# Performance work log

Measured on AMD Instinct MI355X. Metric: run time of the kernel, lower is better.

Reference implementation:

```python
import jax, jax.numpy as jnp
import numpy as np

B, S, E = 2, 2048, 2048
H, G = 16, 4
HD = E // H  # 128 head dim


def setup_inputs() -> dict:
    key = jax.random.key(0)
    k1, k2, k3, k4 = jax.random.split(key, 4)
    x = jax.random.normal(k1, (B, S, E), dtype=jnp.float32)
    mask = jnp.zeros((B, 1, S, S), dtype=jnp.float32)
    # torch nn.Linear weights stored as [in, out] for x @ W
    W1 = jax.random.normal(k2, (E, 2 * G * HD), dtype=jnp.float32) * 0.02
    W2 = jax.random.normal(k3, (E, E), dtype=jnp.float32) * 0.02
    W3 = jax.random.normal(k4, (E, E), dtype=jnp.float32) * 0.02
    return {"x": x, "mask": mask, "W1": W1, "W2": W2, "W3": W3}


def reference(x, mask, W1, W2, W3):
    b, s, e_model = x.shape
    hd = e_model // H
    # linear_1 -> rearrange 'b s (n g e) -> n b g s e'
    kv = (x @ W1).reshape(b, s, 2, G, hd).transpose(2, 0, 3, 1, 4)
    k, v = kv[0], kv[1]  # [b, g, s, e]
    # linear_2 -> 'b t (h e) -> b h t e'
    q = (x @ W2).reshape(b, s, H, hd).transpose(0, 2, 1, 3)  # [b, h, t, e]
    # NOTE: g is summed out here, exactly as in the source einsum (no sqrt scaling)
    score = jnp.einsum('bhte,bgse->bhts', q, k)
    score = jax.nn.softmax(score + mask, axis=-1)
    out = jnp.einsum('bhts,bgse->bthe', score, v)  # g summed again
    out = out.reshape(b, s, e_model)
    return out @ W3
```

## Files before the change

### kernel.cpp

```cpp
#include <hip/hip_runtime.h>
#include <cstdint>

#define S_LEN 2048
#define EMB   2048
#define NHEAD 16
#define HDIM  128
#define NFUSE 2304
#define LOG2E 1.4426950408889634f

typedef __attribute__((ext_vector_type(8))) _Float16 h8;
typedef __attribute__((ext_vector_type(4))) _Float16 h4;
typedef __attribute__((ext_vector_type(8))) short short8;
typedef __attribute__((ext_vector_type(4))) short short4v;
typedef __attribute__((ext_vector_type(4))) float f32x4;
typedef unsigned int u32;

__device__ inline short f2bf(float x) {
  union { float f; uint32_t u; } v; v.f = x;
  uint32_t r = v.u + 0x7fffu + ((v.u >> 16) & 1u);
  return (short)(r >> 16);
}
__device__ inline float bf2f(short b) {
  union { uint32_t u; float f; } v; v.u = ((uint32_t)(uint16_t)b) << 16;
  return v.f;
}
__device__ inline float fexp2(float x) {
  float r;
  __asm__ volatile("v_exp_f32 %0, %1" : "=v"(r) : "v"(x));
  return r;
}
__device__ inline u32 pkrtz(float a, float b) {
  u32 r;
  __asm__ volatile("v_cvt_pkrtz_f16_f32 %0, %1, %2" : "=v"(r) : "v"(a), "v"(b));
  return r;
}
__device__ inline void glds16(const void* g, void* l) {
  __builtin_amdgcn_global_load_lds(
      (const __attribute__((address_space(1))) u32*)g,
      (__attribute__((address_space(3))) u32*)l, 16, 0, 0);
}

__global__ __launch_bounds__(256) void reduce_w1_kernel(
    const float* __restrict__ W1, float* __restrict__ Wkv) {
  int idx = blockIdx.x * 256 + threadIdx.x;
  int i = idx >> 8;
  int c = idx & 255;
  int base = (c < 128) ? c : (c + 384);
  const float* r = W1 + (size_t)i * 1024 + base;
  Wkv[idx] = (r[0] + r[128]) + (r[256] + r[384]);
}

__global__ __launch_bounds__(256) void cvt_x_kernel(
    const float* __restrict__ src, _Float16* __restrict__ dst) {
  size_t idx = (size_t)blockIdx.x * 256 + threadIdx.x;
  float4 v = *(const float4*)(src + idx * 4);
  h4 o;
  o[0] = (_Float16)v.x; o[1] = (_Float16)v.y;
  o[2] = (_Float16)v.z; o[3] = (_Float16)v.w;
  *(h4*)(dst + idx * 4) = o;
}

__global__ __launch_bounds__(256) void cvt_mask_kernel(
    const float* __restrict__ src, short* __restrict__ dst) {
  size_t idx = (size_t)blockIdx.x * 256 + threadIdx.x;
  float4 v = *(const float4*)(src + idx * 4);
  short4v o;
  o[0] = f2bf(v.x * LOG2E); o[1] = f2bf(v.y * LOG2E);
  o[2] = f2bf(v.z * LOG2E); o[3] = f2bf(v.w * LOG2E);
  *(short4v*)(dst + idx * 4) = o;
}

__global__ __launch_bounds__(256) void transpose_f16_kernel(
    const float* __restrict__ W, _Float16* __restrict__ T, int K, int N) {
  __shared__ float Tt[64][65];
  const int tid = threadIdx.x;
  const int k0 = blockIdx.y * 64, n0 = blockIdx.x * 64;
  {
    int r = tid >> 2, c0 = (tid & 3) * 16;
    const float* src = W + (size_t)(k0 + r) * N + n0 + c0;
#pragma unroll
    for (int j = 0; j < 4; ++j) {
      float4 v = *(const float4*)(src + 4 * j);
      Tt[r][c0 + 4 * j + 0] = v.x; Tt[r][c0 + 4 * j + 1] = v.y;
      Tt[r][c0 + 4 * j + 2] = v.z; Tt[r][c0 + 4 * j + 3] = v.w;
    }
  }
  __syncthreads();
  {
    int n = tid >> 2, kc = (tid & 3) * 16;
    h8 o0, o1;
#pragma unroll
    for (int i = 0; i < 8; ++i) {
      o0[i] = (_Float16)Tt[kc + i][n];
      o1[i] = (_Float16)Tt[kc + 8 + i][n];
    }
    size_t off = (size_t)(n0 + n) * K + k0 + kc;
    *(h8*)(T + off) = o0;
    *(h8*)(T + off + 8) = o1;
  }
}

template <bool QSCALE>
__global__ __launch_bounds__(256, 3) void gemm_f16(
    const _Float16* __restrict__ A, const _Float16* __restrict__ Bt,
    float* __restrict__ C, _Float16* __restrict__ Cf,
    int M, int N, int K, int qlim) {
  extern __shared__ char smraw[];
  _Float16* sm = (_Float16*)smraw;
  const int BUFS = 8192;

  const int tid  = threadIdx.x;
  const int w    = tid >> 6;
  const int lane = tid & 63;
  const int quad = lane >> 4, col16 = lane & 15;
  const int row0 = blockIdx.y * 128, col0 = blockIdx.x * 128;
  const float esc = (col0 < qlim) ? LOG2E : 1.0f;

  const int srow  = w * 32 + (lane >> 2);
  const int kpart = (lane & 3) * 8;
  const _Float16* pA0 = A + (size_t)(row0 + srow) * K + kpart;
  const _Float16* pA1 = pA0 + (size_t)16 * K;
  const _Float16* pB0 = Bt + (size_t)(col0 + srow) * K + kpart;
  const _Float16* pB1 = pB0 + (size_t)16 * K;

  const int oA0 = (w * 32) * 32, oA1 = (w * 32 + 16) * 32;
  const int oB0 = 4096 + (w * 32) * 32, oB1 = 4096 + (w * 32 + 16) * 32;

#define STAGE_GEMM(bo)                                                        \
  do {                                                                        \
    glds16(pA0, sm + (bo) + oA0); glds16(pA1, sm + (bo) + oA1);               \
    glds16(pB0, sm + (bo) + oB0); glds16(pB1, sm + (bo) + oB1);               \
    pA0 += 32; pA1 += 32; pB0 += 32; pB1 += 32;                               \
  } while (0)

  f32x4 acc[2][8];
#pragma unroll
  for (int mt = 0; mt < 2; ++mt)
#pragma unroll
    for (int nt = 0; nt < 8; ++nt) {
      acc[mt][nt][0] = 0.f; acc[mt][nt][1] = 0.f;
      acc[mt][nt][2] = 0.f; acc[mt][nt][3] = 0.f;
    }

  const int nchunk = K >> 5;
  int bo = 0;
  STAGE_GEMM(0);

#pragma unroll 1
  for (int c = 0; c < nchunk; ++c) {
    if (c + 1 < nchunk) {
      STAGE_GEMM(bo ^ BUFS);
      __asm__ volatile("s_waitcnt vmcnt(4)" ::: "memory");
    } else {
      __asm__ volatile("s_waitcnt vmcnt(0)" ::: "memory");
    }
    __builtin_amdgcn_s_barrier();

    const _Float16* AS = sm + bo;
    const _Float16* BS = sm + bo + 4096;

    h8 af[2];
#pragma unroll
    for (int mt = 0; mt < 2; ++mt)
      af[mt] = *(const h8*)&AS[(w * 32 + mt * 16 + col16) * 32 + quad * 8];
#pragma unroll
    for (int nt = 0; nt < 8; ++nt) {
      h8 b8 = *(const h8*)&BS[(nt * 16 + col16) * 32 + quad * 8];
#pragma unroll
      for (int mt = 0; mt < 2; ++mt)
        acc[mt][nt] = __builtin_amdgcn_mfma_f32_16x16x32_f16(af[mt], b8, acc[mt][nt], 0, 0, 0);
    }
    __builtin_amdgcn_s_barrier();
    bo ^= BUFS;
  }
#undef STAGE_GEMM

#pragma unroll
  for (int mt = 0; mt < 2; ++mt)
#pragma unroll
    for (int nt = 0; nt < 8; ++nt)
#pragma unroll
      for (int r = 0; r < 4; ++r) {
        int row = row0 + w * 32 + mt * 16 + quad * 4 + r;
        int col = col0 + nt * 16 + col16;
        float v = acc[mt][nt][r];
        if constexpr (QSCALE) {
          Cf[(size_t)row * N + col] = (_Float16)(v * esc);
        } else {
          C[(size_t)row * N + col] = v;
        }
      }
}

__global__ __launch_bounds__(256) void build_vt(
    const short* __restrict__ QKh, short* __restrict__ VT) {
  __shared__ short T[64][136];
  const int tid = threadIdx.x;
  const int gs = blockIdx.x * 64;
  const int b = gs >> 11;
  const int s = gs & 2047;
  {
    int r = tid >> 2, c0 = (tid & 3) * 32;
    const short* src = QKh + (size_t)(gs + r) * NFUSE + 2176 + c0;
#pragma unroll
    for (int j = 0; j < 4; ++j)
      *(short8*)&T[r][c0 + 8 * j] = *(const short8*)(src + 8 * j);
  }
  __syncthreads();
  {
    int d = tid >> 1, c = (tid & 1) * 32;
    short* dst = VT + (size_t)(b * HDIM + d) * S_LEN + s + c;
#pragma unroll
    for (int jo = 0; jo < 4; ++jo) {
      short8 o;
#pragma unroll
      for (int i = 0; i < 8; ++i) o[i] = T[c + jo * 8 + i][d];
      *(short8*)(dst + jo * 8) = o;
    }
  }
}

__global__ __launch_bounds__(256, 2) void flash_f16(
    const _Float16* __restrict__ QKf, const _Float16* __restrict__ VT,
    const short* __restrict__ maskb, _Float16* __restrict__ AO) {
  __shared__ _Float16 KS[64 * 128];
  __shared__ _Float16 VtS[128 * 64];
  __shared__ _Float16 PsS[2 * 4 * 16 * 64];
  __shared__ short    MkS[4 * 32 * 64];

  const int tid   = threadIdx.x;
  const int w     = tid >> 6;
  const int lane  = tid & 63;
  const int quad  = lane >> 4;
  const int col16 = lane & 15;
  const int xq    = col16 & 7;
  const int bh = blockIdx.y, b = bh >> 4, h = bh & 15;
  const int t0 = blockIdx.x * 128;

  const int jr = lane >> 4;
  const int kg = lane & 15;
  const int vr = lane >> 3;
  const int vg = lane & 7;

  _Float16* myK = KS + w * 2048;
  _Float16* myV = VtS + w * 2048;
  short*    myM = MkS + w * 2048;

  h8 qf[2][4];
#pragma unroll
  for (int t = 0; t < 2; ++t) {
#pragma unroll
    for (int j = 0; j < 4; ++j) {
      int rl = 4 * j + jr;
      int gq = kg ^ (rl & 7);
      size_t go = (size_t)(b * S_LEN + t0 + 64 * t + 16 * w + rl) * NFUSE
                + h * HDIM + gq * 8;
      glds16(QKf + go, myK + j * 512);
    }
    __asm__ volatile("s_waitcnt vmcnt(0)" ::: "memory");
#pragma unroll
    for (int c = 0; c < 4; ++c)
      qf[t][c] = *(const h8*)&myK[col16 * 128 + (((c * 4 + quad) ^ xq) * 8)];
    __asm__ volatile("s_waitcnt lgkmcnt(0)" ::: "memory");
  }

  const _Float16* Kbase = QKf + (size_t)b * S_LEN * NFUSE + 2048;
  const _Float16* Vbase = VT + (size_t)b * HDIM * S_LEN;
  const short*    Mbase = maskb + (size_t)b * S_LEN * S_LEN;
  u32 offK[4], offV[4], offM[4];
#pragma unroll
  for (int j = 0; j < 4; ++j) {
    int rl = 4 * j + jr;
    offK[j] = (u32)(16 * w + rl) * NFUSE + (u32)((kg ^ (rl & 7)) * 8);
    int dl = 32 * w + 8 * j + vr;
    offV[j] = (u32)dl * S_LEN + (u32)((vg ^ (vr & 7)) * 8);
    int mrw = j * 8 + (lane >> 3);
    int mq  = t0 + 64 * (mrw >> 4) + 16 * w + (mrw & 15);
    offM[j] = (u32)mq * S_LEN + (u32)(((lane & 7) ^ (mrw & 7)) * 8);
  }

#pragma unroll
  for (int j = 0; j < 4; ++j) glds16(Kbase + offK[j], myK + j * 512);
#pragma unroll
  for (int j = 0; j < 4; ++j) glds16(Mbase + offM[j], myM + j * 512);
#pragma unroll
  for (int j = 0; j < 4; ++j) glds16(Vbase + offV[j], myV + j * 512);
#pragma unroll
  for (int j = 0; j < 4; ++j) {
    offK[j] += 64 * NFUSE; offM[j] += 64; offV[j] += 64;
  }

  f32x4 oacc[2][8];
#pragma unroll
  for (int t = 0; t < 2; ++t)
#pragma unroll
    for (int d = 0; d < 8; ++d) {
      oacc[t][d][0] = 0.f; oacc[t][d][1] = 0.f;
      oacc[t][d][2] = 0.f; oacc[t][d][3] = 0.f;
    }
  float mrow[2] = {-3.0e38f, -3.0e38f};
  float lrow[2] = {0.f, 0.f};

#pragma unroll 1
  for (int it = 0; it < S_LEN / 64; ++it) {
    __asm__ volatile("s_waitcnt vmcnt(8)" ::: "memory");
    __builtin_amdgcn_s_barrier();

    f32x4 sacc[2][4];
#pragma unroll
    for (int t = 0; t < 2; ++t)
#pragma unroll
      for (int nt = 0; nt < 4; ++nt) {
        sacc[t][nt][0] = 0.f; sacc[t][nt][1] = 0.f;
        sacc[t][nt][2] = 0.f; sacc[t][nt][3] = 0.f;
      }
    __builtin_amdgcn_s_setprio(1);
#pragma unroll
    for (int c = 0; c < 4; ++c)
#pragma unroll
      for (int nt = 0; nt < 4; ++nt) {
        h8 k8 = *(const h8*)&KS[(nt * 16 + col16) * 128 + (((c * 4 + quad) ^ xq) * 8)];
#pragma unroll
        for (int t = 0; t < 2; ++t)
          sacc[t][nt] = __builtin_amdgcn_mfma_f32_16x16x32_f16(k8, qf[t][c], sacc[t][nt], 0, 0, 0);
      }
    __builtin_amdgcn_s_setprio(0);

    __asm__ volatile("s_waitcnt vmcnt(0)" ::: "memory");
    short4v msk[2][4];
#pragma unroll
    for (int t = 0; t < 2; ++t)
#pragma unroll
      for (int nt = 0; nt < 4; ++nt)
        msk[t][nt] = *(const short4v*)
            &myM[(t * 16 + col16) * 64 + (((quad + nt * 4) ^ (xq << 1)) << 2)];
    __asm__ volatile("s_waitcnt lgkmcnt(0)" ::: "memory");
    __builtin_amdgcn_s_barrier();

    if (it + 1 < S_LEN / 64) {
#pragma unroll
      for (int j = 0; j < 4; ++j) glds16(Kbase + offK[j], myK + j * 512);
#pragma unroll
      for (int j = 0; j < 4; ++j) glds16(Mbase + offM[j], myM + j * 512);
#pragma unroll
      for (int j = 0; j < 4; ++j) { offK[j] += 64 * NFUSE; offM[j] += 64; }
    }

#pragma unroll
    for (int t = 0; t < 2; ++t) {
      float vv[4][4];
#pragma unroll
      for (int nt = 0; nt < 4; ++nt)
#pragma unroll
        for (int r = 0; r < 4; ++r)
          vv[nt][r] = sacc[t][nt][r] + bf2f(msk[t][nt][r]);
      float mx = vv[0][0];
#pragma unroll
      for (int nt = 0; nt < 4; ++nt)
#pragma unroll
        for (int r = 0; r < 4; ++r) mx = fmaxf(mx, vv[nt][r]);
      mx = fmaxf(mx, __shfl_xor(mx, 16));
      mx = fmaxf(mx, __shfl_xor(mx, 32));

      float nm = fmaxf(mrow[t], mx);
      if (__all(mx - mrow[t] <= 8.0f)) {
        nm = mrow[t];
      } else {
        float al = fexp2(mrow[t] - nm);
        lrow[t] *= al;
#pragma unroll
        for (int d = 0; d < 8; ++d) {
          oacc[t][d][0] *= al; oacc[t][d][1] *= al;
          oacc[t][d][2] *= al; oacc[t][d][3] *= al;
        }
        mrow[t] = nm;
      }

      float ps = 0.f;
      u32 pk0[4], pk1[4];
#pragma unroll
      for (int nt = 0; nt < 4; ++nt) {
        float p0 = fexp2(vv[nt][0] - nm);
        float p1 = fexp2(vv[nt][1] - nm);
        float p2 = fexp2(vv[nt][2] - nm);
        float p3 = fexp2(vv[nt][3] - nm);
        ps += (p0 + p1) + (p2 + p3);
        pk0[nt] = pkrtz(p0, p1);
        pk1[nt] = pkrtz(p2, p3);
      }
      ps += __shfl_xor(ps, 16);
      ps += __shfl_xor(ps, 32);
      lrow[t] += ps;

      int pbase = ((t * 4 + w) * 16 + col16) * 64 + (quad & 1) * 4;
#pragma unroll
      for (int nt = 0; nt < 4; ++nt) {
        uint2 pv2; pv2.x = pk0[nt]; pv2.y = pk1[nt];
        *(uint2*)&PsS[pbase + (((2 * nt + (quad >> 1)) ^ xq) * 8)] = pv2;
      }
    }

    __asm__ volatile("s_waitcnt lgkmcnt(0)" ::: "memory");
    h8 pa[2][2];
#pragma unroll
    for (int t = 0; t < 2; ++t) {
      int pb = ((t * 4 + w) * 16 + col16) * 64;
      pa[t][0] = *(const h8*)&PsS[pb + ((quad ^ xq) * 8)];
      pa[t][1] = *(const h8*)&PsS[pb + (((4 + quad) ^ xq) * 8)];
    }
    __builtin_amdgcn_s_setprio(1);
#pragma unroll
    for (int d = 0; d < 8; ++d) {
      int vo = (d * 16 + col16) * 64;
      h8 vb0 = *(const h8*)&VtS[vo + ((quad ^ xq) * 8)];
      h8 vb1 = *(const h8*)&VtS[vo + (((4 + quad) ^ xq) * 8)];
#pragma unroll
      for (int t = 0; t < 2; ++t) {
        oacc[t][d] = __builtin_amdgcn_mfma_f32_16x16x32_f16(vb0, pa[t][0], oacc[t][d], 0, 0, 0);
        oacc[t][d] = __builtin_amdgcn_mfma_f32_16x16x32_f16(vb1, pa[t][1], oacc[t][d], 0, 0, 0);
      }
    }
    __builtin_amdgcn_s_setprio(0);

    __builtin_amdgcn_s_barrier();
    if (it + 1 < S_LEN / 64) {
#pragma unroll
      for (int j = 0; j < 4; ++j) glds16(Vbase + offV[j], myV + j * 512);
#pragma unroll
      for (int j = 0; j < 4; ++j) offV[j] += 64;
    }
  }

#pragma unroll
  for (int t = 0; t < 2; ++t) {
    float inv = 1.0f / lrow[t];
    int q = t0 + 64 * t + 16 * w + col16;
    _Float16* dst = AO + (size_t)(b * S_LEN + q) * EMB + h * HDIM + quad * 4;
#pragma unroll
    for (int d = 0; d < 8; ++d) {
      h4 o4;
#pragma unroll
      for (int r = 0; r < 4; ++r) o4[r] = (_Float16)(oacc[t][d][r] * inv);
      *(h4*)(dst + d * 16) = o4;
    }
  }
}

extern "C" void kernel_launch(void* const* d_in, const int* in_sizes, int n_in,
                              void* d_out, int out_size, void* d_ws, size_t ws_size,
                              hipStream_t stream) {
  const float* x    = (const float*)d_in[0];
  const float* mask = (const float*)d_in[1];
  const float* W1   = (const float*)d_in[2];
  const float* W2   = (const float*)d_in[3];
  const float* W3   = (const float*)d_in[4];
  float* out = (float*)d_out;

  char* ws = (char*)d_ws;
  size_t off = 0;
  _Float16* xf   = (_Float16*)(ws + off); off += (size_t)4096 * 2048 * 2;
  _Float16* Wtf  = (_Float16*)(ws + off); off += (size_t)NFUSE * 2048 * 2;
  _Float16* QKf  = (_Float16*)(ws + off); off += (size_t)4096 * NFUSE * 2;
  _Float16* VT   = (_Float16*)(ws + off); off += (size_t)2 * 128 * 2048 * 2;
  _Float16* AOf  = (_Float16*)(ws + off); off += (size_t)4096 * 2048 * 2;
  float*    Wkv  = (float*)(ws + off);    off += (size_t)2048 * 256 * 4;
  short*    maskb= (short*)(ws + off);    off += (size_t)2 * 2048 * 2048 * 2;
  _Float16* W3t  = xf;

  reduce_w1_kernel<<<2048, 256, 0, stream>>>(W1, Wkv);
  cvt_x_kernel<<<8192, 256, 0, stream>>>(x, xf);
  cvt_mask_kernel<<<8192, 256, 0, stream>>>(mask, maskb);
  transpose_f16_kernel<<<dim3(32, 32), 256, 0, stream>>>(W2, Wtf, 2048, 2048);
  transpose_f16_kernel<<<dim3(4, 32), 256, 0, stream>>>(
      Wkv, Wtf + (size_t)2048 * 2048, 2048, 256);

  gemm_f16<true><<<dim3(NFUSE / 128, 32), 256, 32768, stream>>>(
      xf, Wtf, nullptr, QKf, 4096, NFUSE, 2048, 2048);

  build_vt<<<64, 256, 0, stream>>>((const short*)QKf, (short*)VT);

  flash_f16<<<dim3(S_LEN / 128, 2 * NHEAD), 256, 0, stream>>>(
      QKf, VT, maskb, AOf);

  transpose_f16_kernel<<<dim3(32, 32), 256, 0, stream>>>(W3, W3t, 2048, 2048);
  gemm_f16<false><<<dim3(16, 32), 256, 32768, stream>>>(
      AOf, W3t, out, nullptr, 4096, 2048, 2048, 0);
}
```

Before: 365.7 us.

## Interleave per-tile softmax with PV MFMAs and hoist mask load before QK

Restructures the attention inner loop so the softmax for the second 16-row tile runs after the first tile's PV MFMAs, and K/V fragments are held in registers and reused across both tiles. The mask LDS read moves ahead of the QK MFMAs, and the vmcnt waits are retuned to match the new order of async loads. The goal is to overlap VALU exp/max work with matrix-core work and cut LDS re-reads. In exchange, register pressure rises from holding the kreg and vreg arrays, which could lower occupancy or cause spills.

```diff
diff --git a/kernel.cpp b/kernel.cpp
--- a/kernel.cpp
+++ b/kernel.cpp
@@ -301,10 +301,71 @@
   float mrow[2] = {-3.0e38f, -3.0e38f};
   float lrow[2] = {0.f, 0.f};
 
+#define SOFTMAX_TILE(T)                                                       \
+  {                                                                           \
+    float vv[4][4];                                                           \
+    _Pragma("unroll")                                                         \
+    for (int nt = 0; nt < 4; ++nt) {                                          \
+      _Pragma("unroll")                                                       \
+      for (int r = 0; r < 4; ++r)                                             \
+        vv[nt][r] = sacc[T][nt][r] + bf2f(msk[T][nt][r]);                     \
+    }                                                                         \
+    float mx = vv[0][0];                                                      \
+    _Pragma("unroll")                                                         \
+    for (int nt = 0; nt < 4; ++nt) {                                          \
+      _Pragma("unroll")                                                       \
+      for (int r = 0; r < 4; ++r) mx = fmaxf(mx, vv[nt][r]);                  \
+    }                                                                         \
+    mx = fmaxf(mx, __shfl_xor(mx, 16));                                       \
+    mx = fmaxf(mx, __shfl_xor(mx, 32));                                       \
+    float nm = fmaxf(mrow[T], mx);                                            \
+    if (__all(mx - mrow[T] <= 8.0f)) {                                        \
+      nm = mrow[T];                                                           \
+    } else {                                                                  \
+      float al = fexp2(mrow[T] - nm);                                         \
+      lrow[T] *= al;                                                          \
+      _Pragma("unroll")                                                       \
+      for (int d = 0; d < 8; ++d) {                                           \
+        oacc[T][d][0] *= al; oacc[T][d][1] *= al;                             \
+        oacc[T][d][2] *= al; oacc[T][d][3] *= al;                             \
+      }                                                                       \
+      mrow[T] = nm;                                                           \
+    }                                                                         \
+    float ps = 0.f;                                                           \
+    u32 pk0[4], pk1[4];                                                       \
+    _Pragma("unroll")                                                         \
+    for (int nt = 0; nt < 4; ++nt) {                                          \
+      float p0 = fexp2(vv[nt][0] - nm);                                       \
+      float p1 = fexp2(vv[nt][1] - nm);                                       \
+      float p2 = fexp2(vv[nt][2] - nm);                                       \
+      float p3 = fexp2(vv[nt][3] - nm);                                       \
+      ps += (p0 + p1) + (p2 + p3);                                            \
+      pk0[nt] = pkrtz(p0, p1);                                                \
+      pk1[nt] = pkrtz(p2, p3);                                                \
+    }                                                                         \
+    ps += __shfl_xor(ps, 16);                                                 \
+    ps += __shfl_xor(ps, 32);                                                 \
+    lrow[T] += ps;                                                            \
+    int pbase = ((T * 4 + w) * 16 + col16) * 64 + (quad & 1) * 4;             \
+    _Pragma("unroll")                                                         \
+    for (int nt = 0; nt < 4; ++nt) {                                          \
+      uint2 pv2; pv2.x = pk0[nt]; pv2.y = pk1[nt];                            \
+      *(uint2*)&PsS[pbase + (((2 * nt + (quad >> 1)) ^ xq) * 8)] = pv2;       \
+    }                                                                         \
+  }
+
 #pragma unroll 1
   for (int it = 0; it < S_LEN / 64; ++it) {
-    __asm__ volatile("s_waitcnt vmcnt(8)" ::: "memory");
+    __asm__ volatile("s_waitcnt vmcnt(4)" ::: "memory");
     __builtin_amdgcn_s_barrier();
+
+    short4v msk[2][4];
+#pragma unroll
+    for (int t = 0; t < 2; ++t)
+#pragma unroll
+      for (int nt = 0; nt < 4; ++nt)
+        msk[t][nt] = *(const short4v*)
+            &myM[(t * 16 + col16) * 64 + (((quad + nt * 4) ^ (xq << 1)) << 2)];
 
     f32x4 sacc[2][4];
 #pragma unroll
@@ -314,29 +375,24 @@
         sacc[t][nt][0] = 0.f; sacc[t][nt][1] = 0.f;
         sacc[t][nt][2] = 0.f; sacc[t][nt][3] = 0.f;
       }
+    h8 kreg[4][4];
     __builtin_amdgcn_s_setprio(1);
 #pragma unroll
     for (int c = 0; c < 4; ++c)
 #pragma unroll
       for (int nt = 0; nt < 4; ++nt) {
-        h8 k8 = *(const h8*)&KS[(nt * 16 + col16) * 128 + (((c * 4 + quad) ^ xq) * 8)];
-#pragma unroll
-        for (int t = 0; t < 2; ++t)
-          sacc[t][nt] = __builtin_amdgcn_mfma_f32_16x16x32_f16(k8, qf[t][c], sacc[t][nt], 0, 0, 0);
+        kreg[c][nt] = *(const h8*)&KS[(nt * 16 + col16) * 128 + (((c * 4 + quad) ^ xq) * 8)];
+        sacc[0][nt] = __builtin_amdgcn_mfma_f32_16x16x32_f16(kreg[c][nt], qf[0][c], sacc[0][nt], 0, 0, 0);
       }
+#pragma unroll
+    for (int c = 0; c < 4; ++c)
+#pragma unroll
+      for (int nt = 0; nt < 4; ++nt)
+        sacc[1][nt] = __builtin_amdgcn_mfma_f32_16x16x32_f16(kreg[c][nt], qf[1][c], sacc[1][nt], 0, 0, 0);
     __builtin_amdgcn_s_setprio(0);
 
-    __asm__ volatile("s_waitcnt vmcnt(0)" ::: "memory");
-    short4v msk[2][4];
-#pragma unroll
-    for (int t = 0; t < 2; ++t)
-#pragma unroll
-      for (int nt = 0; nt < 4; ++nt)
-        msk[t][nt] = *(const short4v*)
-            &myM[(t * 16 + col16) * 64 + (((quad + nt * 4) ^ (xq << 1)) << 2)];
     __asm__ volatile("s_waitcnt lgkmcnt(0)" ::: "memory");
     __builtin_amdgcn_s_barrier();
-
     if (it + 1 < S_LEN / 64) {
 #pragma unroll
       for (int j = 0; j < 4; ++j) glds16(Kbase + offK[j], myK + j * 512);
@@ -346,82 +402,50 @@
       for (int j = 0; j < 4; ++j) { offK[j] += 64 * NFUSE; offM[j] += 64; }
     }
 
-#pragma unroll
-    for (int t = 0; t < 2; ++t) {
-      float vv[4][4];
-#pragma unroll
-      for (int nt = 0; nt < 4; ++nt)
-#pragma unroll
-        for (int r = 0; r < 4; ++r)
-          vv[nt][r] = sacc[t][nt][r] + bf2f(msk[t][nt][r]);
-      float mx = vv[0][0];
-#pragma unroll
-      for (int nt = 0; nt < 4; ++nt)
-#pragma unroll
-        for (int r = 0; r < 4; ++r) mx = fmaxf(mx, vv[nt][r]);
-      mx = fmaxf(mx, __shfl_xor(mx, 16));
-      mx = fmaxf(mx, __shfl_xor(mx, 32));
-
-      float nm = fmaxf(mrow[t], mx);
-      if (__all(mx - mrow[t] <= 8.0f)) {
-        nm = mrow[t];
-      } else {
-        float al = fexp2(mrow[t] - nm);
-        lrow[t] *= al;
-#pragma unroll
-        for (int d = 0; d < 8; ++d) {
-          oacc[t][d][0] *= al; oacc[t][d][1] *= al;
-          oacc[t][d][2] *= al; oacc[t][d][3] *= al;
-        }
-        mrow[t] = nm;
-      }
-
-      float ps = 0.f;
-      u32 pk0[4], pk1[4];
-#pragma unroll
-      for (int nt = 0; nt < 4; ++nt) {
-        float p0 = fexp2(vv[nt][0] - nm);
-        float p1 = fexp2(vv[nt][1] - nm);
-        float p2 = fexp2(vv[nt][2] - nm);
-        float p3 = fexp2(vv[nt][3] - nm);
-        ps += (p0 + p1) + (p2 + p3);
-        pk0[nt] = pkrtz(p0, p1);
-        pk1[nt] = pkrtz(p2, p3);
-      }
-      ps += __shfl_xor(ps, 16);
-      ps += __shfl_xor(ps, 32);
-      lrow[t] += ps;
-
-      int pbase = ((t * 4 + w) * 16 + col16) * 64 + (quad & 1) * 4;
-#pragma unroll
-      for (int nt = 0; nt < 4; ++nt) {
-        uint2 pv2; pv2.x = pk0[nt]; pv2.y = pk1[nt];
-        *(uint2*)&PsS[pbase + (((2 * nt + (quad >> 1)) ^ xq) * 8)] = pv2;
-      }
-    }
-
+    SOFTMAX_TILE(0)
+
+    if (it + 1 < S_LEN / 64) {
+      __asm__ volatile("s_waitcnt vmcnt(8)" ::: "memory");
+    } else {
+      __asm__ volatile("s_waitcnt vmcnt(0)" ::: "memory");
+    }
     __asm__ volatile("s_waitcnt lgkmcnt(0)" ::: "memory");
-    h8 pa[2][2];
-#pragma unroll
-    for (int t = 0; t < 2; ++t) {
-      int pb = ((t * 4 + w) * 16 + col16) * 64;
-      pa[t][0] = *(const h8*)&PsS[pb + ((quad ^ xq) * 8)];
-      pa[t][1] = *(const h8*)&PsS[pb + (((4 + quad) ^ xq) * 8)];
-    }
+
+    h8 pa0[2];
+    {
+      int pb = ((0 * 4 + w) * 16 + col16) * 64;
+      pa0[0] = *(const h8*)&PsS[pb + ((quad ^ xq) * 8)];
+      pa0[1] = *(const h8*)&PsS[pb + (((4 + quad) ^ xq) * 8)];
+    }
+    h8 vreg[8][2];
     __builtin_amdgcn_s_setprio(1);
 #pragma unroll
     for (int d = 0; d < 8; ++d) {
       int vo = (d * 16 + col16) * 64;
-      h8 vb0 = *(const h8*)&VtS[vo + ((quad ^ xq) * 8)];
-      h8 vb1 = *(const h8*)&VtS[vo + (((4 + quad) ^ xq) * 8)];
-#pragma unroll
-      for (int t = 0; t < 2; ++t) {
-        oacc[t][d] = __builtin_amdgcn_mfma_f32_16x16x32_f16(vb0, pa[t][0], oacc[t][d], 0, 0, 0);
-        oacc[t][d] = __builtin_amdgcn_mfma_f32_16x16x32_f16(vb1, pa[t][1], oacc[t][d], 0, 0, 0);
-      }
+      vreg[d][0] = *(const h8*)&VtS[vo + ((quad ^ xq) * 8)];
+      vreg[d][1] = *(const h8*)&VtS[vo + (((4 + quad) ^ xq) * 8)];
+      oacc[0][d] = __builtin_amdgcn_mfma_f32_16x16x32_f16(vreg[d][0], pa0[0], oacc[0][d], 0, 0, 0);
+      oacc[0][d] = __builtin_amdgcn_mfma_f32_16x16x32_f16(vreg[d][1], pa0[1], oacc[0][d], 0, 0, 0);
     }
     __builtin_amdgcn_s_setprio(0);
 
+    SOFTMAX_TILE(1)
+    __asm__ volatile("s_waitcnt lgkmcnt(0)" ::: "memory");
+    h8 pa1[2];
+    {
+      int pb = ((1 * 4 + w) * 16 + col16) * 64;
+      pa1[0] = *(const h8*)&PsS[pb + ((quad ^ xq) * 8)];
+      pa1[1] = *(const h8*)&PsS[pb + (((4 + quad) ^ xq) * 8)];
+    }
+    __builtin_amdgcn_s_setprio(1);
+#pragma unroll
+    for (int d = 0; d < 8; ++d) {
+      oacc[1][d] = __builtin_amdgcn_mfma_f32_16x16x32_f16(vreg[d][0], pa1[0], oacc[1][d], 0, 0, 0);
+      oacc[1][d] = __builtin_amdgcn_mfma_f32_16x16x32_f16(vreg[d][1], pa1[1], oacc[1][d], 0, 0, 0);
+    }
+    __builtin_amdgcn_s_setprio(0);
+
+    __asm__ volatile("s_waitcnt lgkmcnt(0)" ::: "memory");
     __builtin_amdgcn_s_barrier();
     if (it + 1 < S_LEN / 64) {
 #pragma unroll
@@ -430,6 +454,7 @@
       for (int j = 0; j < 4; ++j) offV[j] += 64;
     }
   }
+#undef SOFTMAX_TILE
 
 #pragma unroll
   for (int t = 0; t < 2; ++t) {
```

Result: no change. 370.7 us (+1.4%).

## Fuse preprocessing kernels and remap GEMM workgroups for XCD locality

Applied to the files above, without the earlier changes.

Merges the x and mask conversion kernels into one launch and folds the W1 group reduction into the transpose kernel, removing a launch and the intermediate Wkv buffer round trip. The GEMM also remaps workgroup IDs so that consecutive tiles land on the same XCD, aiming for better L2 reuse of A/B tiles. The remap assumes the grid size is divisible by 8.

```diff
diff --git a/kernel.cpp b/kernel.cpp
--- a/kernel.cpp
+++ b/kernel.cpp
@@ -40,34 +40,25 @@
       (__attribute__((address_space(3))) u32*)l, 16, 0, 0);
 }
 
-__global__ __launch_bounds__(256) void reduce_w1_kernel(
-    const float* __restrict__ W1, float* __restrict__ Wkv) {
-  int idx = blockIdx.x * 256 + threadIdx.x;
-  int i = idx >> 8;
-  int c = idx & 255;
-  int base = (c < 128) ? c : (c + 384);
-  const float* r = W1 + (size_t)i * 1024 + base;
-  Wkv[idx] = (r[0] + r[128]) + (r[256] + r[384]);
-}
-
-__global__ __launch_bounds__(256) void cvt_x_kernel(
-    const float* __restrict__ src, _Float16* __restrict__ dst) {
-  size_t idx = (size_t)blockIdx.x * 256 + threadIdx.x;
-  float4 v = *(const float4*)(src + idx * 4);
-  h4 o;
-  o[0] = (_Float16)v.x; o[1] = (_Float16)v.y;
-  o[2] = (_Float16)v.z; o[3] = (_Float16)v.w;
-  *(h4*)(dst + idx * 4) = o;
-}
-
-__global__ __launch_bounds__(256) void cvt_mask_kernel(
-    const float* __restrict__ src, short* __restrict__ dst) {
-  size_t idx = (size_t)blockIdx.x * 256 + threadIdx.x;
-  float4 v = *(const float4*)(src + idx * 4);
-  short4v o;
-  o[0] = f2bf(v.x * LOG2E); o[1] = f2bf(v.y * LOG2E);
-  o[2] = f2bf(v.z * LOG2E); o[3] = f2bf(v.w * LOG2E);
-  *(short4v*)(dst + idx * 4) = o;
+__global__ __launch_bounds__(256) void cvt_xm_kernel(
+    const float* __restrict__ x, _Float16* __restrict__ xf,
+    const float* __restrict__ mask, short* __restrict__ maskb) {
+  int bid = blockIdx.x;
+  if (bid < 8192) {
+    size_t idx = (size_t)bid * 256 + threadIdx.x;
+    float4 v = *(const float4*)(x + idx * 4);
+    h4 o;
+    o[0] = (_Float16)v.x; o[1] = (_Float16)v.y;
+    o[2] = (_Float16)v.z; o[3] = (_Float16)v.w;
+    *(h4*)(xf + idx * 4) = o;
+  } else {
+    size_t idx = (size_t)(bid - 8192) * 256 + threadIdx.x;
+    float4 v = *(const float4*)(mask + idx * 4);
+    short4v o;
+    o[0] = f2bf(v.x * LOG2E); o[1] = f2bf(v.y * LOG2E);
+    o[2] = f2bf(v.z * LOG2E); o[3] = f2bf(v.w * LOG2E);
+    *(short4v*)(maskb + idx * 4) = o;
+  }
 }
 
 __global__ __launch_bounds__(256) void transpose_f16_kernel(
@@ -100,6 +91,42 @@
   }
 }
 
+__global__ __launch_bounds__(256) void transpose_wkv_kernel(
+    const float* __restrict__ W1, _Float16* __restrict__ T) {
+  __shared__ float Tt[64][65];
+  const int tid = threadIdx.x;
+  const int k0 = blockIdx.y * 64, n0 = blockIdx.x * 64;
+  {
+    int r = tid >> 2, c0 = (tid & 3) * 16;
+    int base = n0 + c0 + ((n0 >= 128) ? 384 : 0);
+    const float* src = W1 + (size_t)(k0 + r) * 1024 + base;
+#pragma unroll
+    for (int j = 0; j < 4; ++j) {
+      float4 s0 = *(const float4*)(src + 4 * j);
+      float4 s1 = *(const float4*)(src + 128 + 4 * j);
+      float4 s2 = *(const float4*)(src + 256 + 4 * j);
+      float4 s3 = *(const float4*)(src + 384 + 4 * j);
+      Tt[r][c0 + 4 * j + 0] = (s0.x + s1.x) + (s2.x + s3.x);
+      Tt[r][c0 + 4 * j + 1] = (s0.y + s1.y) + (s2.y + s3.y);
+      Tt[r][c0 + 4 * j + 2] = (s0.z + s1.z) + (s2.z + s3.z);
+      Tt[r][c0 + 4 * j + 3] = (s0.w + s1.w) + (s2.w + s3.w);
+    }
+  }
+  __syncthreads();
+  {
+    int n = tid >> 2, kc = (tid & 3) * 16;
+    h8 o0, o1;
+#pragma unroll
+    for (int i = 0; i < 8; ++i) {
+      o0[i] = (_Float16)Tt[kc + i][n];
+      o1[i] = (_Float16)Tt[kc + 8 + i][n];
+    }
+    size_t off = (size_t)(n0 + n) * 2048 + k0 + kc;
+    *(h8*)(T + off) = o0;
+    *(h8*)(T + off + 8) = o1;
+  }
+}
+
 template <bool QSCALE>
 __global__ __launch_bounds__(256, 3) void gemm_f16(
     const _Float16* __restrict__ A, const _Float16* __restrict__ Bt,
@@ -113,7 +140,14 @@
   const int w    = tid >> 6;
   const int lane = tid & 63;
   const int quad = lane >> 4, col16 = lane & 15;
-  const int row0 = blockIdx.y * 128, col0 = blockIdx.x * 128;
+
+  const int nwgx = gridDim.x;
+  const int id   = blockIdx.y * nwgx + blockIdx.x;
+  const int cpx  = (nwgx * gridDim.y) >> 3;
+  const int sid  = (id & 7) * cpx + (id >> 3);
+  const int bx   = sid % nwgx, by = sid / nwgx;
+
+  const int row0 = by * 128, col0 = bx * 128;
   const float esc = (col0 < qlim) ? LOG2E : 1.0f;
 
   const int srow  = w * 32 + (lane >> 2);
@@ -463,16 +497,13 @@
   _Float16* QKf  = (_Float16*)(ws + off); off += (size_t)4096 * NFUSE * 2;
   _Float16* VT   = (_Float16*)(ws + off); off += (size_t)2 * 128 * 2048 * 2;
   _Float16* AOf  = (_Float16*)(ws + off); off += (size_t)4096 * 2048 * 2;
-  float*    Wkv  = (float*)(ws + off);    off += (size_t)2048 * 256 * 4;
   short*    maskb= (short*)(ws + off);    off += (size_t)2 * 2048 * 2048 * 2;
   _Float16* W3t  = xf;
 
-  reduce_w1_kernel<<<2048, 256, 0, stream>>>(W1, Wkv);
-  cvt_x_kernel<<<8192, 256, 0, stream>>>(x, xf);
-  cvt_mask_kernel<<<8192, 256, 0, stream>>>(mask, maskb);
+  cvt_xm_kernel<<<16384, 256, 0, stream>>>(x, xf, mask, maskb);
   transpose_f16_kernel<<<dim3(32, 32), 256, 0, stream>>>(W2, Wtf, 2048, 2048);
-  transpose_f16_kernel<<<dim3(4, 32), 256, 0, stream>>>(
-      Wkv, Wtf + (size_t)2048 * 2048, 2048, 256);
+  transpose_wkv_kernel<<<dim3(4, 32), 256, 0, stream>>>(
+      W1, Wtf + (size_t)2048 * 2048);
 
   gemm_f16<true><<<dim3(NFUSE / 128, 32), 256, 32768, stream>>>(
       xf, Wtf, nullptr, QKf, 4096, NFUSE, 2048, 2048);
```

Measured after the change: 346.5 us. 1.06x faster.
